# Optimization experiments

Hardware: AMD Instinct MI355X
Metric: run time of the kernel (lower is better)

The kernel has to match this reference:

```python
import jax, jax.numpy as jnp
import numpy as np

G = 8    # deformable groups
K2 = 9   # 3x3 kernel taps


def conv3(x, w, b=None):
    # 3x3, stride 1, SAME padding, NCHW
    y = jax.lax.conv_general_dilated(x, w, (1, 1), 'SAME',
                                     dimension_numbers=('NCHW', 'OIHW', 'NCHW'))
    if b is not None:
        y = y + b[None, :, None, None]
    return y


def deform_conv(x, offset, wgt):
    # DCNv1: x [B,C,H,W], offset [B, G*K2*2, H, W] (per tap: dy,dx), wgt [O,C,3,3]
    B, C, H, W = x.shape
    Cpg = C // G
    off = offset.reshape(B, G, K2, 2, H, W)
    dy, dx = off[:, :, :, 0], off[:, :, :, 1]                      # [B,G,K2,H,W]
    ky = jnp.repeat(jnp.arange(-1, 2), 3).astype(x.dtype)          # tap row offsets
    kx = jnp.tile(jnp.arange(-1, 2), 3).astype(x.dtype)            # tap col offsets
    py = dy + jnp.arange(H, dtype=x.dtype)[None, None, None, :, None] + ky[None, None, :, None, None]
    px = dx + jnp.arange(W, dtype=x.dtype)[None, None, None, None, :] + kx[None, None, :, None, None]
    xg = x.reshape(B, G, Cpg, H * W)
    y0 = jnp.floor(py)
    x0 = jnp.floor(px)

    def corner(yc, xc):
        m = ((yc >= 0) & (yc <= H - 1) & (xc >= 0) & (xc <= W - 1)).astype(x.dtype)
        yi = jnp.clip(yc, 0, H - 1).astype(jnp.int32)
        xi = jnp.clip(xc, 0, W - 1).astype(jnp.int32)
        idx = (yi * W + xi).reshape(B, G, -1)                      # [B,G,K2*H*W]
        v = jax.vmap(jax.vmap(lambda f, i: f[:, i]))(xg, idx)      # [B,G,Cpg,K2*H*W]
        return v.reshape(B, G, Cpg, K2, H, W), m

    v00, m00 = corner(y0, x0)
    v01, m01 = corner(y0, x0 + 1)
    v10, m10 = corner(y0 + 1, x0)
    v11, m11 = corner(y0 + 1, x0 + 1)
    wy = py - y0
    wx = px - x0
    w00 = ((1 - wy) * (1 - wx) * m00)[:, :, None]   # [B,G,1,K2,H,W]
    w01 = ((1 - wy) * wx * m01)[:, :, None]
    w10 = (wy * (1 - wx) * m10)[:, :, None]
    w11 = (wy * wx * m11)[:, :, None]
    sampled = v00 * w00 + v01 * w01 + v10 * w10 + v11 * w11        # [B,G,Cpg,K2,H,W]
    O = wgt.shape[0]
    return jnp.einsum('bgckhw,ogck->bohw', sampled, wgt.reshape(O, G, Cpg, K2))


def setup_inputs() -> dict:
    key = jax.random.key(0)
    ks = jax.random.split(key, 16)

    def he(k, shape):
        # torch init: normal(0, sqrt(2 / (kh*kw*out_ch)))
        o = shape[-4]
        return jax.random.normal(k, shape, jnp.float32) * np.float32(np.sqrt(2.0 / (9 * o)))

    inp = {
        'x': jax.random.normal(ks[0], (2, 5, 3, 128, 128), jnp.float32),
        'conv_first_w': he(ks[1], (64, 3, 3, 3)),
        'conv_first_b': jax.random.normal(ks[2], (64,), jnp.float32) * 0.01,
        'res_w1': he(ks[3], (5, 64, 64, 3, 3)),
        'res_b1': jax.random.normal(ks[4], (5, 64), jnp.float32) * 0.01,
        'res_w2': he(ks[5], (5, 64, 64, 3, 3)),
        'res_b2': jax.random.normal(ks[6], (5, 64), jnp.float32) * 0.01,
        'cr_w': he(ks[7], (64, 128, 3, 3)),
        'cr_b': jax.random.normal(ks[8], (64,), jnp.float32) * 0.01,
        'off_w': he(ks[9], (4, 144, 64, 3, 3)),
        'off_b': jax.random.normal(ks[10], (4, 144), jnp.float32) * 0.01,
        'dconv_w': he(ks[11], (4, 64, 64, 3, 3)),
        'recon_w': he(ks[12], (3, 64, 3, 3)),
        'recon_b': jax.random.normal(ks[13], (3,), jnp.float32) * 0.01,
    }
    return inp


def reference(x, conv_first_w, conv_first_b, res_w1, res_b1, res_w2, res_b2,
              cr_w, cr_b, off_w, off_b, dconv_w, recon_w, recon_b):
    B, N, C, H, W = x.shape
    center = N // 2
    # shared feature trunk over all frames
    out = jax.nn.relu(conv3(x.reshape(B * N, C, H, W), conv_first_w, conv_first_b))
    for i in range(res_w1.shape[0]):
        r = jax.nn.relu(conv3(out, res_w1[i], res_b1[i]))
        out = out + conv3(r, res_w2[i], res_b2[i])
    out = out.reshape(B, N, 64, H, W)
    ref = out[:, center]                                   # [B,64,H,W]
    supp_idx = np.array([i for i in range(N) if i != center])
    supp = out[:, supp_idx].reshape(B * (N - 1), 64, H, W)
    ref_rep = jnp.broadcast_to(ref[:, None], (B, N - 1, 64, H, W)).reshape(B * (N - 1), 64, H, W)
    # alignment cascade (vectorized over the N-1 support frames)
    fea = conv3(jnp.concatenate([ref_rep, supp], axis=1), cr_w, cr_b)
    fea = deform_conv(fea, conv3(fea, off_w[0], off_b[0]), dconv_w[0])
    fea = deform_conv(fea, conv3(fea, off_w[1], off_b[1]), dconv_w[1])
    fea = deform_conv(supp, conv3(fea, off_w[2], off_b[2]), dconv_w[2])
    aligned = deform_conv(fea, conv3(fea, off_w[3], off_b[3]), dconv_w[3])
    im = conv3(aligned, recon_w, recon_b)                  # [B*(N-1),3,H,W]
    ims = im.reshape(B, N - 1, 3, H, W)
    feas = fea.reshape(B, N - 1, 64, H, W)
    x_center = x[:, center]
    lrs = jnp.concatenate([ims[:, :center], x_center[:, None], ims[:, center:]], axis=1)
    feats = jnp.concatenate([feas[:, :center], ref[:, None], feas[:, center:]], axis=1)
    return lrs, feats
```

## Files before the change

### kernel.cpp

```cpp
#include <hip/hip_runtime.h>

#define HH 128
#define WW 128
#define HWX (HH*WW)

using f32x4 = __attribute__((ext_vector_type(4))) float;
using f16x8 = __attribute__((ext_vector_type(8))) _Float16;

__device__ __forceinline__ unsigned short f16bits(_Float16 h) {
  union { _Float16 f; unsigned short u; } v; v.f = h; return v.u;
}

__device__ __forceinline__ int swz(int pos, int q) {
  return pos * 32 + (((q + pos + (pos >> 2)) & 3) << 3);
}

__global__ __launch_bounds__(256) void wprep_k(
    const float* __restrict__ src, unsigned short* __restrict__ dhi,
    unsigned short* __restrict__ dlo, int O, int I, int L)
{
  int idx = blockIdx.x * 256 + threadIdx.x;
  int tot = L * O * I * 9;
  if (idx >= tot) return;
  int per = O * I * 9;
  int layer = idx / per;
  int r = idx - layer * per;
  int o = r / (I * 9);
  int r2 = r - o * (I * 9);
  int i = r2 / 9, k = r2 - i * 9;
  float v = src[idx];
  _Float16 h = (_Float16)v;
  _Float16 l = (_Float16)(v - (float)h);
  long di = (long)layer * per + ((long)k * O + o) * I + i;
  dhi[di] = f16bits(h);
  dlo[di] = f16bits(l);
}

__global__ __launch_bounds__(256) void dwprep_k(
    const float* __restrict__ src, unsigned short* __restrict__ dhi,
    unsigned short* __restrict__ dlo)
{
  int idx = blockIdx.x * 256 + threadIdx.x;
  if (idx >= 147456) return;
  int l = idx / 36864;
  int rem = idx - l * 36864;
  int o = rem / 576;
  int rem2 = rem - o * 576;
  int r = rem2 / 9, k2 = rem2 - r * 9;
  float v = src[idx];
  _Float16 h = (_Float16)v;
  _Float16 lo = (_Float16)(v - (float)h);
  long di = (((long)l * 9 + k2) * 64 + o) * 64 + r;
  dhi[di] = f16bits(h);
  dlo[di] = f16bits(lo);
}

template<int CBLK, int NFRAG, bool RELU, bool ADD, bool CRMODE>
__global__ __launch_bounds__(256, 3) void conv_mfma_k(
    const float* __restrict__ in, const unsigned short* __restrict__ whi,
    const unsigned short* __restrict__ wlo,
    const float* __restrict__ bias, const float* __restrict__ res,
    float* __restrict__ out, int Cout, int nslice, int img_in0, int img_out0)
{
  constexpr int CIN = CBLK * 32;
  constexpr int OCB = NFRAG * 16;
  constexpr int SLAB = OCB * 32;
  __shared__ __align__(16) unsigned short s_in[2 * 10880];
  __shared__ __align__(16) unsigned short s_w[2 * SLAB];

  const int tid = threadIdx.x;
  const int lane = tid & 63;
  const int wv = tid >> 6;
  const int m16 = lane & 15, q = lane >> 4;
  const int iz = blockIdx.z / nslice, slice = blockIdx.z % nslice;
  const int oc_blk0 = slice * OCB;
  const int x0 = blockIdx.x * 32, y0 = blockIdx.y * 8;

  f32x4 acc[4][NFRAG];
#pragma unroll
  for (int mt = 0; mt < 4; ++mt)
#pragma unroll
    for (int nt = 0; nt < NFRAG; ++nt)
#pragma unroll
      for (int i = 0; i < 4; ++i) acc[mt][nt][i] = 0.f;

  int bb = 0, nn = 0;
  const float* inb = in;
  if (CRMODE) {
    int j = img_in0 + iz;
    bb = j >> 2;
    int ns = j & 3;
    nn = ns < 2 ? ns : ns + 1;
  } else {
    inb = in + (long)(img_in0 + iz) * CIN * HWX;
  }

  for (int cb = 0; cb < CBLK; ++cb) {
    const int c0 = cb * 32;
    if (cb > 0) __syncthreads();
    for (int t = tid; t < 1360; t += 256) {
      int qq = t / 340, pos = t - qq * 340;
      int iy = pos / 34, ix = pos - iy * 34;
      int gy = y0 + iy - 1, gx = x0 + ix - 1;
      bool inr = (gy >= 0 && gy < HH && gx >= 0 && gx < WW);
      const float* src;
      if (CRMODE) {
        int ch = c0 + qq * 8;
        int simg = (ch < 64) ? (bb * 5 + 2) : (bb * 5 + nn);
        src = in + ((long)simg * 64 + (ch & 63)) * HWX + gy * WW + gx;
      } else {
        src = inb + (long)(c0 + qq * 8) * HWX + gy * WW + gx;
      }
      unsigned hi4[4], lo4[4];
#pragma unroll
      for (int j2 = 0; j2 < 4; ++j2) {
        unsigned short hs[2], ls[2];
#pragma unroll
        for (int j = 0; j < 2; ++j) {
          float v = inr ? src[(long)(j2 * 2 + j) * HWX] : 0.f;
          _Float16 h = (_Float16)v;
          _Float16 l = (_Float16)(v - (float)h);
          hs[j] = f16bits(h); ls[j] = f16bits(l);
        }
        hi4[j2] = (unsigned)hs[0] | ((unsigned)hs[1] << 16);
        lo4[j2] = (unsigned)ls[0] | ((unsigned)ls[1] << 16);
      }
      *(uint4*)(s_in + swz(pos, qq)) = make_uint4(hi4[0], hi4[1], hi4[2], hi4[3]);
      *(uint4*)(s_in + 10880 + swz(pos, qq)) =
          make_uint4(lo4[0], lo4[1], lo4[2], lo4[3]);
    }
    for (int t = tid; t < OCB * 4; t += 256) {
      int qq = t & 3, ocl = t >> 2;
      long so = ((long)0 * Cout + oc_blk0 + ocl) * CIN + c0 + qq * 8;
      *(uint4*)(s_w + swz(ocl, qq)) = *(const uint4*)(whi + so);
      *(uint4*)(s_w + SLAB + swz(ocl, qq)) = *(const uint4*)(wlo + so);
    }
    __syncthreads();

#pragma unroll
    for (int kp = 0; kp < 9; ++kp) {
      uint4 sth, stl;
      int sd = -1;
      if (kp < 8 && tid < OCB * 4) {
        int qq = tid & 3, ocl = tid >> 2;
        long so = ((long)(kp + 1) * Cout + oc_blk0 + ocl) * CIN + c0 + qq * 8;
        sth = *(const uint4*)(whi + so);
        stl = *(const uint4*)(wlo + so);
        sd = swz(ocl, qq);
      }
      const int dy = kp / 3, dx = kp - dy * 3;
      f16x8 bhi[NFRAG], blo[NFRAG];
#pragma unroll
      for (int nt = 0; nt < NFRAG; ++nt) {
        int pw = nt * 16 + m16;
        bhi[nt] = *(const f16x8*)(s_w + swz(pw, q));
        blo[nt] = *(const f16x8*)(s_w + SLAB + swz(pw, q));
      }
#pragma unroll
      for (int mt = 0; mt < 4; ++mt) {
        int r = 2 * wv + (mt >> 1), h = mt & 1;
        int pos = (r + dy) * 34 + h * 16 + m16 + dx;
        f16x8 ahi = *(const f16x8*)(s_in + swz(pos, q));
        f16x8 alo = *(const f16x8*)(s_in + 10880 + swz(pos, q));
#pragma unroll
        for (int nt = 0; nt < NFRAG; ++nt) {
          acc[mt][nt] = __builtin_amdgcn_mfma_f32_16x16x32_f16(
              ahi, blo[nt], acc[mt][nt], 0, 0, 0);
          acc[mt][nt] = __builtin_amdgcn_mfma_f32_16x16x32_f16(
              alo, bhi[nt], acc[mt][nt], 0, 0, 0);
          acc[mt][nt] = __builtin_amdgcn_mfma_f32_16x16x32_f16(
              ahi, bhi[nt], acc[mt][nt], 0, 0, 0);
        }
      }
      if (kp < 8) {
        __syncthreads();
        if (sd >= 0) {
          *(uint4*)(s_w + sd) = sth;
          *(uint4*)(s_w + SLAB + sd) = stl;
        }
        __syncthreads();
      }
    }
  }

  const int img_o = img_out0 + iz;
#pragma unroll
  for (int mt = 0; mt < 4; ++mt) {
    int r = 2 * wv + (mt >> 1), h = mt & 1;
    int y = y0 + r;
    int xb = x0 + h * 16 + q * 4;
#pragma unroll
    for (int nt = 0; nt < NFRAG; ++nt) {
      int oc = oc_blk0 + nt * 16 + m16;
      if (oc < Cout) {
        float bsv = bias[oc];
        long base = ((long)img_o * Cout + oc) * HWX + (long)y * WW + xb;
#pragma unroll
        for (int i = 0; i < 4; ++i) {
          float v = acc[mt][nt][i] + bsv;
          if (RELU) v = fmaxf(v, 0.f);
          if (ADD) v += res[base + i];
          out[base + i] = v;
        }
      }
    }
  }
}

template<int CIN, int CK, int OCB, bool RELU, bool ADD>
__global__ __launch_bounds__(256) void conv3x3_k(
    const float* __restrict__ in, const float* __restrict__ wgt,
    const float* __restrict__ bias, const float* __restrict__ res,
    float* __restrict__ out, int Cout, int nslice, int img_in0, int img_out0)
{
  __shared__ __align__(16) float s_in[CK][34][34];
  __shared__ __align__(16) float s_w[CK * 9 * OCB];

  const int tid = threadIdx.x;
  const int tx = tid & 31;
  const int ty = tid >> 5;
  const int iz = blockIdx.z / nslice;
  const int slice = blockIdx.z % nslice;
  const int oc0 = slice * OCB;
  const int x0 = blockIdx.x * 32;
  const int y0 = blockIdx.y * 32;

  float acc[4][OCB];
#pragma unroll
  for (int r = 0; r < 4; ++r)
#pragma unroll
    for (int o = 0; o < OCB; ++o) acc[r][o] = 0.f;

  const float* inb = in + (long)(img_in0 + iz) * CIN * HWX;

  for (int c0 = 0; c0 < CIN; c0 += CK) {
    __syncthreads();
    for (int idx = tid; idx < CK * 34 * 34; idx += 256) {
      int c = idx / 1156;
      int rem = idx % 1156;
      int iy = rem / 34, ix = rem % 34;
      int gy = y0 + iy - 1, gx = x0 + ix - 1;
      float v = 0.f;
      if (gy >= 0 && gy < HH && gx >= 0 && gx < WW)
        v = inb[(long)(c0 + c) * HWX + gy * WW + gx];
      s_in[c][iy][ix] = v;
    }
    for (int idx = tid; idx < CK * 9 * OCB; idx += 256) {
      int oc = idx % OCB;
      int ck = idx / OCB;
      int c = ck / 9, k = ck % 9;
      int ocg = oc0 + oc;
      float v = 0.f;
      if (ocg < Cout) v = wgt[((long)ocg * CIN + c0 + c) * 9 + k];
      s_w[idx] = v;
    }
    __syncthreads();

    for (int c = 0; c < CK; ++c) {
#pragma unroll
      for (int k = 0; k < 9; ++k) {
        const int ky = k / 3, kx = k % 3;
        float v0 = s_in[c][ty + ky][tx + kx];
        float v1 = s_in[c][ty + 8 + ky][tx + kx];
        float v2 = s_in[c][ty + 16 + ky][tx + kx];
        float v3 = s_in[c][ty + 24 + ky][tx + kx];
        const float4* wp = (const float4*)&s_w[(c * 9 + k) * OCB];
#pragma unroll
        for (int o4 = 0; o4 < OCB / 4; ++o4) {
          float4 w4 = wp[o4];
          acc[0][o4 * 4 + 0] += v0 * w4.x; acc[0][o4 * 4 + 1] += v0 * w4.y;
          acc[0][o4 * 4 + 2] += v0 * w4.z; acc[0][o4 * 4 + 3] += v0 * w4.w;
          acc[1][o4 * 4 + 0] += v1 * w4.x; acc[1][o4 * 4 + 1] += v1 * w4.y;
          acc[1][o4 * 4 + 2] += v1 * w4.z; acc[1][o4 * 4 + 3] += v1 * w4.w;
          acc[2][o4 * 4 + 0] += v2 * w4.x; acc[2][o4 * 4 + 1] += v2 * w4.y;
          acc[2][o4 * 4 + 2] += v2 * w4.z; acc[2][o4 * 4 + 3] += v2 * w4.w;
          acc[3][o4 * 4 + 0] += v3 * w4.x; acc[3][o4 * 4 + 1] += v3 * w4.y;
          acc[3][o4 * 4 + 2] += v3 * w4.z; acc[3][o4 * 4 + 3] += v3 * w4.w;
        }
      }
    }
  }

#pragma unroll
  for (int o = 0; o < OCB; ++o) {
    int ocg = oc0 + o;
    if (ocg < Cout) {
      float b = bias ? bias[ocg] : 0.f;
      long base = ((long)(img_out0 + iz) * Cout + ocg) * HWX;
#pragma unroll
      for (int r = 0; r < 4; ++r) {
        int y = y0 + ty + 8 * r;
        float v = acc[r][o] + b;
        if (RELU) v = fmaxf(v, 0.f);
        long ia = base + (long)y * WW + x0 + tx;
        if (ADD) v += res[ia];
        out[ia] = v;
      }
    }
  }
}

__global__ __launch_bounds__(256) void regroup_k(
    const float* __restrict__ src, float* __restrict__ dst, int supp_mode)
{
  int idx = blockIdx.x * 256 + threadIdx.x;
  int c = idx & 7;
  int p = (idx >> 3) & 16383;
  int g = (idx >> 17) & 7;
  int img = idx >> 20;
  int simg = img;
  if (supp_mode) {
    int b = img >> 2, ns = img & 3;
    simg = b * 5 + (ns < 2 ? ns : ns + 1);
  }
  dst[idx] = src[((simg * 64 + g * 8 + c) * HWX) + p];
}

__global__ __launch_bounds__(256) void deform_mfma_k(
    const float* __restrict__ srcg, const float* __restrict__ off,
    const unsigned short* __restrict__ wh, const unsigned short* __restrict__ wl,
    float* __restrict__ out, int img0, int cmask, int cshift)
{
  __shared__ __align__(16) unsigned short s_w[2][2 * 4096];
  const int tid = threadIdx.x;
  const int lane = tid & 63;
  const int wv = tid >> 6;
  const int m16 = lane & 15, q = lane >> 4;
  const int bid = blockIdx.x;
  const int iz = bid & cmask;
  const int tile = bid >> cshift;
  const int img = img0 + iz;
  const int tp0 = tile * 64;
  const int p = tp0 + wv * 16 + m16;
  const float fy = (float)(p >> 7), fx = (float)(p & 127);
  const int rot = 8 * (m16 & 7);

  const float* offb = off + (long)iz * 144 * HWX + p;
  const float* sgq[2];
  sgq[0] = srcg + (long)(img * 8 + q) * HWX * 8;
  sgq[1] = srcg + (long)(img * 8 + 4 + q) * HWX * 8;

  float dyr[3], dxr[3];
  float pyr[2], pxr[2];
  float4 cr[2][8];

#define LOAD_OFF(T, SLOT) { \
    const float* ob_ = offb + ((long)(4 * ((T) & 1) + q) * 18 + 2 * ((T) >> 1)) * HWX; \
    dyr[SLOT] = ob_[0]; dxr[SLOT] = ob_[HWX]; }

#define ISSUE(T, SLOT, OS) { \
    const int k2_ = (T) >> 1; \
    float py_ = dyr[OS] + fy + (float)(k2_ / 3 - 1); \
    float px_ = dxr[OS] + fx + (float)(k2_ % 3 - 1); \
    pyr[SLOT] = py_; pxr[SLOT] = px_; \
    float y0f_ = floorf(py_), x0f_ = floorf(px_); \
    int yi0_ = (int)fminf(fmaxf(y0f_, 0.f), 127.f); \
    int yi1_ = (int)fminf(fmaxf(y0f_ + 1.f, 0.f), 127.f); \
    int xi0_ = (int)fminf(fmaxf(x0f_, 0.f), 127.f); \
    int xi1_ = (int)fminf(fmaxf(x0f_ + 1.f, 0.f), 127.f); \
    const float* sg_ = sgq[(T) & 1]; \
    const float4* p00_ = (const float4*)(sg_ + ((long)yi0_ * WW + xi0_) * 8); \
    const float4* p01_ = (const float4*)(sg_ + ((long)yi0_ * WW + xi1_) * 8); \
    const float4* p10_ = (const float4*)(sg_ + ((long)yi1_ * WW + xi0_) * 8); \
    const float4* p11_ = (const float4*)(sg_ + ((long)yi1_ * WW + xi1_) * 8); \
    cr[SLOT][0] = p00_[0]; cr[SLOT][1] = p00_[1]; \
    cr[SLOT][2] = p01_[0]; cr[SLOT][3] = p01_[1]; \
    cr[SLOT][4] = p10_[0]; cr[SLOT][5] = p10_[1]; \
    cr[SLOT][6] = p11_[0]; cr[SLOT][7] = p11_[1]; }

#define STAGE(K2) { \
    const int buf_ = (K2) & 1; \
    for (int t2 = tid; t2 < 512; t2 += 256) { \
      int o_ = t2 >> 3, j_ = t2 & 7; \
      int d_ = o_ * 64 + ((8 * j_ + 8 * (o_ & 7)) & 63); \
      long so_ = ((long)(K2) * 64 + o_) * 64 + 8 * j_; \
      *(uint4*)(s_w[buf_] + d_) = *(const uint4*)(wh + so_); \
      *(uint4*)(s_w[buf_] + 4096 + d_) = *(const uint4*)(wl + so_); \
    } }

#define PROCESS(T, SLOT) { \
    float py_ = pyr[SLOT], px_ = pxr[SLOT]; \
    float y0f_ = floorf(py_), x0f_ = floorf(px_); \
    float wy_ = py_ - y0f_, wx_ = px_ - x0f_; \
    float my0 = (y0f_ >= 0.f && y0f_ <= 127.f) ? 1.f : 0.f; \
    float my1 = (y0f_ >= -1.f && y0f_ <= 126.f) ? 1.f : 0.f; \
    float mx0 = (x0f_ >= 0.f && x0f_ <= 127.f) ? 1.f : 0.f; \
    float mx1 = (x0f_ >= -1.f && x0f_ <= 126.f) ? 1.f : 0.f; \
    float w00 = (1.f - wy_) * (1.f - wx_) * my0 * mx0; \
    float w01 = (1.f - wy_) * wx_ * my0 * mx1; \
    float w10 = wy_ * (1.f - wx_) * my1 * mx0; \
    float w11 = wy_ * wx_ * my1 * mx1; \
    f16x8 ah, al; \
    _Pragma("unroll") \
    for (int j = 0; j < 4; ++j) { \
      float v0 = w00 * ((const float*)&cr[SLOT][0])[j] + w01 * ((const float*)&cr[SLOT][2])[j] \
               + w10 * ((const float*)&cr[SLOT][4])[j] + w11 * ((const float*)&cr[SLOT][6])[j]; \
      float v1 = w00 * ((const float*)&cr[SLOT][1])[j] + w01 * ((const float*)&cr[SLOT][3])[j] \
               + w10 * ((const float*)&cr[SLOT][5])[j] + w11 * ((const float*)&cr[SLOT][7])[j]; \
      _Float16 h0 = (_Float16)v0; ah[j] = h0; al[j] = (_Float16)(v0 - (float)h0); \
      _Float16 h1 = (_Float16)v1; ah[4 + j] = h1; al[4 + j] = (_Float16)(v1 - (float)h1); \
    } \
    const unsigned short* wb_ = s_w[((T) >> 1) & 1]; \
    const int roff_ = (32 * ((T) & 1) + 8 * q + rot) & 63; \
    _Pragma("unroll") \
    for (int nt = 0; nt < 4; ++nt) { \
      int o_ = nt * 16 + m16; \
      f16x8 bh = *(const f16x8*)(wb_ + o_ * 64 + roff_); \
      f16x8 bl = *(const f16x8*)(wb_ + 4096 + o_ * 64 + roff_); \
      acc[nt] = __builtin_amdgcn_mfma_f32_16x16x32_f16(ah, bl, acc[nt], 0, 0, 0); \
      acc[nt] = __builtin_amdgcn_mfma_f32_16x16x32_f16(al, bh, acc[nt], 0, 0, 0); \
      acc[nt] = __builtin_amdgcn_mfma_f32_16x16x32_f16(ah, bh, acc[nt], 0, 0, 0); \
    } }

  f32x4 acc[4];
#pragma unroll
  for (int nt = 0; nt < 4; ++nt)
#pragma unroll
    for (int i = 0; i < 4; ++i) acc[nt][i] = 0.f;

  LOAD_OFF(0, 0);
  LOAD_OFF(1, 1);
  ISSUE(0, 0, 0);
  LOAD_OFF(2, 2);
  STAGE(0);
  __syncthreads();

#pragma unroll
  for (int k2 = 0; k2 < 9; ++k2) {
    if (k2 < 8) STAGE(k2 + 1);
#pragma unroll
    for (int s = 0; s < 2; ++s) {
      const int t = 2 * k2 + s;
      if (t < 17) ISSUE(t + 1, (t + 1) & 1, (t + 1) % 3);
      if (t < 15) LOAD_OFF(t + 3, (t + 3) % 3);
      PROCESS(t, t & 1);
    }
    __syncthreads();
  }

#undef LOAD_OFF
#undef ISSUE
#undef STAGE
#undef PROCESS

  const long pb = tp0 + wv * 16 + q * 4;
#pragma unroll
  for (int nt = 0; nt < 4; ++nt) {
    int oc = nt * 16 + m16;
    float4 v;
    v.x = acc[nt][0]; v.y = acc[nt][1]; v.z = acc[nt][2]; v.w = acc[nt][3];
    *(float4*)(out + ((long)img * 64 + oc) * HWX + pb) = v;
  }
}

__global__ __launch_bounds__(256) void assemble_k(
    const float* __restrict__ x, const float* __restrict__ im,
    const float* __restrict__ out0, const float* __restrict__ fea,
    float* __restrict__ out)
{
  int idx = blockIdx.x * 256 + threadIdx.x;
  if (idx < 491520) {
    int within = idx % 49152;
    int n = (idx / 49152) % 5;
    int b = idx / (49152 * 5);
    float v;
    if (n == 2) v = x[(b * 5 + 2) * 49152 + within];
    else {
      int j = b * 4 + (n < 2 ? n : n - 1);
      v = im[j * 49152 + within];
    }
    out[idx] = v;
  } else if (idx < 10977280) {
    int idx2 = idx - 491520;
    int within = idx2 % 1048576;
    int n = (idx2 / 1048576) % 5;
    int b = idx2 / (1048576 * 5);
    float v;
    if (n == 2) v = out0[(b * 5 + 2) * 1048576 + within];
    else {
      int j = b * 4 + (n < 2 ? n : n - 1);
      v = fea[j * 1048576 + within];
    }
    out[idx] = v;
  }
}

extern "C" void kernel_launch(void* const* d_in, const int* in_sizes, int n_in,
                              void* d_out, int out_size, void* d_ws, size_t ws_size,
                              hipStream_t stream) {
  const float* x   = (const float*)d_in[0];
  const float* cfw = (const float*)d_in[1];
  const float* cfb = (const float*)d_in[2];
  const float* rw1 = (const float*)d_in[3];
  const float* rb1 = (const float*)d_in[4];
  const float* rw2 = (const float*)d_in[5];
  const float* rb2 = (const float*)d_in[6];
  const float* crw = (const float*)d_in[7];
  const float* crb = (const float*)d_in[8];
  const float* ofw = (const float*)d_in[9];
  const float* ofb = (const float*)d_in[10];
  const float* dcw = (const float*)d_in[11];
  const float* rcw = (const float*)d_in[12];
  const float* rcb = (const float*)d_in[13];
  float* out = (float*)d_out;

  unsigned short* WH = (unsigned short*)d_ws;
  unsigned short* WL = WH + 774144;
  unsigned short* DH = WH + 1548288;
  unsigned short* DL = DH + 147456;
  const long W_res1 = 0, W_res2 = 184320, W_cr = 368640, W_off = 442368;

  float* A = (float*)d_ws + 921600;
  float* C = A + 10485760;
  float* D = C + 8388608;
  float* F = D + 8388608;
  float* OFF = F + 8388608;
  float* r = C;
  float* im = D;

  const size_t fixedF = 921600UL + 10485760UL + 3UL * 8388608UL;
  int chunk = 8;
  while (chunk > 1 && (fixedF + (size_t)chunk * 2359296UL) * sizeof(float) > ws_size)
    chunk >>= 1;
  int cshift = (chunk == 8) ? 3 : (chunk == 4) ? 2 : (chunk == 2) ? 1 : 0;

  dim3 blk(256);

  wprep_k<<<720, blk, 0, stream>>>(rw1, WH + W_res1, WL + W_res1, 64, 64, 5);
  wprep_k<<<720, blk, 0, stream>>>(rw2, WH + W_res2, WL + W_res2, 64, 64, 5);
  wprep_k<<<288, blk, 0, stream>>>(crw, WH + W_cr, WL + W_cr, 64, 128, 1);
  wprep_k<<<1296, blk, 0, stream>>>(ofw, WH + W_off, WL + W_off, 144, 64, 4);
  dwprep_k<<<576, blk, 0, stream>>>(dcw, DH, DL);

  conv3x3_k<3, 3, 16, true, false><<<dim3(4, 4, 40), blk, 0, stream>>>(
      x, cfw, cfb, nullptr, A, 64, 4, 0, 0);

  for (int i = 0; i < 5; ++i) {
    conv_mfma_k<2, 4, true, false, false><<<dim3(4, 16, 10), blk, 0, stream>>>(
        A, WH + W_res1 + (long)i * 36864, WL + W_res1 + (long)i * 36864,
        rb1 + i * 64, nullptr, r, 64, 1, 0, 0);
    conv_mfma_k<2, 4, false, true, false><<<dim3(4, 16, 10), blk, 0, stream>>>(
        r, WH + W_res2 + (long)i * 36864, WL + W_res2 + (long)i * 36864,
        rb2 + i * 64, A, A, 64, 1, 0, 0);
  }

  conv_mfma_k<4, 4, false, false, true><<<dim3(4, 16, 8), blk, 0, stream>>>(
      A, WH + W_cr, WL + W_cr, crb, nullptr, C, 64, 1, 0, 0);

  auto off_deform = [&](const float* fea_in, const float* grouped,
                        int layer, float* outp) {
    for (int i0 = 0; i0 < 8; i0 += chunk) {
      conv_mfma_k<2, 3, false, false, false>
          <<<dim3(4, 16, chunk * 3), blk, 0, stream>>>(
              fea_in, WH + W_off + (long)layer * 82944,
              WL + W_off + (long)layer * 82944, ofb + layer * 144,
              nullptr, OFF, 144, 3, i0, 0);
      deform_mfma_k<<<dim3(256 * chunk), blk, 0, stream>>>(
          grouped, OFF, DH + (long)layer * 36864, DL + (long)layer * 36864,
          outp, i0, chunk - 1, cshift);
    }
  };

  regroup_k<<<32768, blk, 0, stream>>>(C, D, 0);
  off_deform(C, D, 0, C);

  regroup_k<<<32768, blk, 0, stream>>>(C, D, 0);
  off_deform(C, D, 1, C);

  regroup_k<<<32768, blk, 0, stream>>>(A, D, 1);
  off_deform(C, D, 2, F);

  regroup_k<<<32768, blk, 0, stream>>>(F, D, 0);
  off_deform(F, D, 3, C);

  conv3x3_k<64, 8, 4, false, false><<<dim3(4, 4, 8), blk, 0, stream>>>(
      C, rcw, rcb, nullptr, im, 3, 1, 0, 0);

  assemble_k<<<42880, blk, 0, stream>>>(x, im, A, F, out);
}
```

Baseline: 1.828 ms.

## Store residual-trunk activations pre-split into fp16 hi/lo in channel-interleaved layout

Producer convolutions in the residual trunk now also write their outputs as fp16 hi/lo pairs in a [C/8][HW][8] interleaved layout. Consumer MFMA convs read these directly with 16-byte vector loads instead of loading eight strided fp32 values and splitting them in the staging loop. This cuts global load count and the per-element conversion work in the input staging. In exchange, producers issue scalar strided 2-byte writes, and the fp32 copy is still written where later stages need it.

Result: faster. 1.773 ms (-3.0%).

```diff
diff --git a/kernel.cpp b/kernel.cpp
--- a/kernel.cpp
+++ b/kernel.cpp
@@ -55,12 +55,14 @@
   dlo[di] = f16bits(lo);
 }
 
-template<int CBLK, int NFRAG, bool RELU, bool ADD, bool CRMODE>
+template<int CBLK, int NFRAG, bool RELU, bool ADD, bool CRMODE, bool SIN, int SOUT>
 __global__ __launch_bounds__(256, 3) void conv_mfma_k(
-    const float* __restrict__ in, const unsigned short* __restrict__ whi,
-    const unsigned short* __restrict__ wlo,
+    const float* __restrict__ in, const unsigned short* __restrict__ inlo,
+    const unsigned short* __restrict__ whi, const unsigned short* __restrict__ wlo,
     const float* __restrict__ bias, const float* __restrict__ res,
-    float* __restrict__ out, int Cout, int nslice, int img_in0, int img_out0)
+    float* __restrict__ out, unsigned short* __restrict__ outh,
+    unsigned short* __restrict__ outl,
+    int Cout, int nslice, int img_in0, int img_out0)
 {
   constexpr int CIN = CBLK * 32;
   constexpr int OCB = NFRAG * 16;
@@ -86,13 +88,20 @@
 
   int bb = 0, nn = 0;
   const float* inb = in;
+  const unsigned short* inb_h = (const unsigned short*)in;
+  const unsigned short* inb_l = inlo;
   if (CRMODE) {
     int j = img_in0 + iz;
     bb = j >> 2;
     int ns = j & 3;
     nn = ns < 2 ? ns : ns + 1;
   } else {
-    inb = in + (long)(img_in0 + iz) * CIN * HWX;
+    if (SIN) {
+      inb_h += (long)(img_in0 + iz) * CIN * HWX;
+      inb_l += (long)(img_in0 + iz) * CIN * HWX;
+    } else {
+      inb = in + (long)(img_in0 + iz) * CIN * HWX;
+    }
   }
 
   for (int cb = 0; cb < CBLK; ++cb) {
@@ -103,31 +112,51 @@
       int iy = pos / 34, ix = pos - iy * 34;
       int gy = y0 + iy - 1, gx = x0 + ix - 1;
       bool inr = (gy >= 0 && gy < HH && gx >= 0 && gx < WW);
-      const float* src;
-      if (CRMODE) {
-        int ch = c0 + qq * 8;
-        int simg = (ch < 64) ? (bb * 5 + 2) : (bb * 5 + nn);
-        src = in + ((long)simg * 64 + (ch & 63)) * HWX + gy * WW + gx;
+      if (SIN) {
+        uint4 hv = make_uint4(0u, 0u, 0u, 0u), lv = make_uint4(0u, 0u, 0u, 0u);
+        if (inr) {
+          long a;
+          if (CRMODE) {
+            int ch = c0 + qq * 8;
+            int simg = (ch < 64) ? (bb * 5 + 2) : (bb * 5 + nn);
+            a = ((long)(simg * 8 + ((ch & 63) >> 3)) * HWX + gy * WW + gx) * 8;
+            hv = *(const uint4*)((const unsigned short*)in + a);
+            lv = *(const uint4*)(inlo + a);
+          } else {
+            a = (long)(c0 + qq * 8) * HWX + (long)(gy * WW + gx) * 8;
+            hv = *(const uint4*)(inb_h + a);
+            lv = *(const uint4*)(inb_l + a);
+          }
+        }
+        *(uint4*)(s_in + swz(pos, qq)) = hv;
+        *(uint4*)(s_in + 10880 + swz(pos, qq)) = lv;
       } else {
-        src = inb + (long)(c0 + qq * 8) * HWX + gy * WW + gx;
-      }
-      unsigned hi4[4], lo4[4];
-#pragma unroll
-      for (int j2 = 0; j2 < 4; ++j2) {
-        unsigned short hs[2], ls[2];
-#pragma unroll
-        for (int j = 0; j < 2; ++j) {
-          float v = inr ? src[(long)(j2 * 2 + j) * HWX] : 0.f;
-          _Float16 h = (_Float16)v;
-          _Float16 l = (_Float16)(v - (float)h);
-          hs[j] = f16bits(h); ls[j] = f16bits(l);
-        }
-        hi4[j2] = (unsigned)hs[0] | ((unsigned)hs[1] << 16);
-        lo4[j2] = (unsigned)ls[0] | ((unsigned)ls[1] << 16);
-      }
-      *(uint4*)(s_in + swz(pos, qq)) = make_uint4(hi4[0], hi4[1], hi4[2], hi4[3]);
-      *(uint4*)(s_in + 10880 + swz(pos, qq)) =
-          make_uint4(lo4[0], lo4[1], lo4[2], lo4[3]);
+        const float* src;
+        if (CRMODE) {
+          int ch = c0 + qq * 8;
+          int simg = (ch < 64) ? (bb * 5 + 2) : (bb * 5 + nn);
+          src = in + ((long)simg * 64 + (ch & 63)) * HWX + gy * WW + gx;
+        } else {
+          src = inb + (long)(c0 + qq * 8) * HWX + gy * WW + gx;
+        }
+        unsigned hi4[4], lo4[4];
+#pragma unroll
+        for (int j2 = 0; j2 < 4; ++j2) {
+          unsigned short hs[2], ls[2];
+#pragma unroll
+          for (int j = 0; j < 2; ++j) {
+            float v = inr ? src[(long)(j2 * 2 + j) * HWX] : 0.f;
+            _Float16 h = (_Float16)v;
+            _Float16 l = (_Float16)(v - (float)h);
+            hs[j] = f16bits(h); ls[j] = f16bits(l);
+          }
+          hi4[j2] = (unsigned)hs[0] | ((unsigned)hs[1] << 16);
+          lo4[j2] = (unsigned)ls[0] | ((unsigned)ls[1] << 16);
+        }
+        *(uint4*)(s_in + swz(pos, qq)) = make_uint4(hi4[0], hi4[1], hi4[2], hi4[3]);
+        *(uint4*)(s_in + 10880 + swz(pos, qq)) =
+            make_uint4(lo4[0], lo4[1], lo4[2], lo4[3]);
+      }
     }
     for (int t = tid; t < OCB * 4; t += 256) {
       int qq = t & 3, ocl = t >> 2;
@@ -195,23 +224,34 @@
       if (oc < Cout) {
         float bsv = bias[oc];
         long base = ((long)img_o * Cout + oc) * HWX + (long)y * WW + xb;
+        long gbase = 0;
+        if (SOUT)
+          gbase = (long)img_o * Cout * HWX + (long)(oc >> 3) * HWX * 8 +
+                  ((long)y * WW + xb) * 8 + (oc & 7);
 #pragma unroll
         for (int i = 0; i < 4; ++i) {
           float v = acc[mt][nt][i] + bsv;
           if (RELU) v = fmaxf(v, 0.f);
           if (ADD) v += res[base + i];
-          out[base + i] = v;
-        }
-      }
-    }
-  }
-}
-
-template<int CIN, int CK, int OCB, bool RELU, bool ADD>
+          if (SOUT) {
+            _Float16 hh = (_Float16)v;
+            outh[gbase + (long)i * 8] = f16bits(hh);
+            outl[gbase + (long)i * 8] = f16bits((_Float16)(v - (float)hh));
+          }
+          if (SOUT != 1) out[base + i] = v;
+        }
+      }
+    }
+  }
+}
+
+template<int CIN, int CK, int OCB, bool RELU, bool ADD, int SOUT>
 __global__ __launch_bounds__(256) void conv3x3_k(
     const float* __restrict__ in, const float* __restrict__ wgt,
     const float* __restrict__ bias, const float* __restrict__ res,
-    float* __restrict__ out, int Cout, int nslice, int img_in0, int img_out0)
+    float* __restrict__ out, unsigned short* __restrict__ outh,
+    unsigned short* __restrict__ outl,
+    int Cout, int nslice, int img_in0, int img_out0)
 {
   __shared__ __align__(16) float s_in[CK][34][34];
   __shared__ __align__(16) float s_w[CK * 9 * OCB];
@@ -294,6 +334,13 @@
         if (RELU) v = fmaxf(v, 0.f);
         long ia = base + (long)y * WW + x0 + tx;
         if (ADD) v += res[ia];
+        if (SOUT) {
+          long ga = (long)(img_out0 + iz) * Cout * HWX + (long)(ocg >> 3) * HWX * 8 +
+                    ((long)y * WW + x0 + tx) * 8 + (ocg & 7);
+          _Float16 hh = (_Float16)v;
+          outh[ga] = f16bits(hh);
+          outl[ga] = f16bits((_Float16)(v - (float)hh));
+        }
         out[ia] = v;
       }
     }
@@ -515,8 +562,12 @@
   float* D = C + 8388608;
   float* F = D + 8388608;
   float* OFF = F + 8388608;
-  float* r = C;
   float* im = D;
+
+  unsigned short* Rh = (unsigned short*)C;
+  unsigned short* Rl = Rh + 10485760;
+  unsigned short* Ah = (unsigned short*)F;
+  unsigned short* Al = Ah + 10485760;
 
   const size_t fixedF = 921600UL + 10485760UL + 3UL * 8388608UL;
   int chunk = 8;
@@ -532,29 +583,30 @@
   wprep_k<<<1296, blk, 0, stream>>>(ofw, WH + W_off, WL + W_off, 144, 64, 4);
   dwprep_k<<<576, blk, 0, stream>>>(dcw, DH, DL);
 
-  conv3x3_k<3, 3, 16, true, false><<<dim3(4, 4, 40), blk, 0, stream>>>(
-      x, cfw, cfb, nullptr, A, 64, 4, 0, 0);
+  conv3x3_k<3, 3, 16, true, false, 2><<<dim3(4, 4, 40), blk, 0, stream>>>(
+      x, cfw, cfb, nullptr, A, Ah, Al, 64, 4, 0, 0);
 
   for (int i = 0; i < 5; ++i) {
-    conv_mfma_k<2, 4, true, false, false><<<dim3(4, 16, 10), blk, 0, stream>>>(
-        A, WH + W_res1 + (long)i * 36864, WL + W_res1 + (long)i * 36864,
-        rb1 + i * 64, nullptr, r, 64, 1, 0, 0);
-    conv_mfma_k<2, 4, false, true, false><<<dim3(4, 16, 10), blk, 0, stream>>>(
-        r, WH + W_res2 + (long)i * 36864, WL + W_res2 + (long)i * 36864,
-        rb2 + i * 64, A, A, 64, 1, 0, 0);
-  }
-
-  conv_mfma_k<4, 4, false, false, true><<<dim3(4, 16, 8), blk, 0, stream>>>(
-      A, WH + W_cr, WL + W_cr, crb, nullptr, C, 64, 1, 0, 0);
+    conv_mfma_k<2, 4, true, false, false, true, 1><<<dim3(4, 16, 10), blk, 0, stream>>>(
+        (const float*)Ah, Al, WH + W_res1 + (long)i * 36864, WL + W_res1 + (long)i * 36864,
+        rb1 + i * 64, nullptr, nullptr, Rh, Rl, 64, 1, 0, 0);
+    conv_mfma_k<2, 4, false, true, false, true, 2><<<dim3(4, 16, 10), blk, 0, stream>>>(
+        (const float*)Rh, Rl, WH + W_res2 + (long)i * 36864, WL + W_res2 + (long)i * 36864,
+        rb2 + i * 64, A, A, Ah, Al, 64, 1, 0, 0);
+  }
+
+  conv_mfma_k<4, 4, false, false, true, true, 0><<<dim3(4, 16, 8), blk, 0, stream>>>(
+      (const float*)Ah, Al, WH + W_cr, WL + W_cr, crb, nullptr, C, nullptr, nullptr,
+      64, 1, 0, 0);
 
   auto off_deform = [&](const float* fea_in, const float* grouped,
                         int layer, float* outp) {
     for (int i0 = 0; i0 < 8; i0 += chunk) {
-      conv_mfma_k<2, 3, false, false, false>
+      conv_mfma_k<2, 3, false, false, false, false, 0>
           <<<dim3(4, 16, chunk * 3), blk, 0, stream>>>(
-              fea_in, WH + W_off + (long)layer * 82944,
+              fea_in, nullptr, WH + W_off + (long)layer * 82944,
               WL + W_off + (long)layer * 82944, ofb + layer * 144,
-              nullptr, OFF, 144, 3, i0, 0);
+              nullptr, OFF, nullptr, nullptr, 144, 3, i0, 0);
       deform_mfma_k<<<dim3(256 * chunk), blk, 0, stream>>>(
           grouped, OFF, DH + (long)layer * 36864, DL + (long)layer * 36864,
           outp, i0, chunk - 1, cshift);
@@ -573,8 +625,8 @@
   regroup_k<<<32768, blk, 0, stream>>>(F, D, 0);
   off_deform(F, D, 3, C);
 
-  conv3x3_k<64, 8, 4, false, false><<<dim3(4, 4, 8), blk, 0, stream>>>(
-      C, rcw, rcb, nullptr, im, 3, 1, 0, 0);
+  conv3x3_k<64, 8, 4, false, false, 0><<<dim3(4, 4, 8), blk, 0, stream>>>(
+      C, rcw, rcb, nullptr, im, nullptr, nullptr, 3, 1, 0, 0);
 
   assemble_k<<<42880, blk, 0, stream>>>(x, im, A, F, out);
 }
```
